# Optimization experiments

Hardware: AMD Instinct MI355X
Metric: run time of the kernel (lower is better)

## Reference

```python
import jax, jax.numpy as jnp
import numpy as np

EPS = 1e-6
NUM_HEADS = 8
FOCUS = 3.0


def setup_inputs() -> dict:
    key = jax.random.key(0)
    ks = jax.random.split(key, 8)
    B, N, C = 16, 4096, 256
    head_dim, ksz = C // NUM_HEADS, 5
    s = 1.0 / np.sqrt(C)
    return {
        "x": jax.random.normal(ks[0], (B, N, C), jnp.float32),
        "Wq": jax.random.normal(ks[1], (C, C), jnp.float32) * s,
        "Wkv": jax.random.normal(ks[2], (C, 2 * C), jnp.float32) * s,
        "Wp": jax.random.normal(ks[3], (C, C), jnp.float32) * s,
        "bp": jnp.zeros((C,), jnp.float32),
        "scale_param": jnp.zeros((1, 1, C), jnp.float32),
        "pos_enc": jax.random.normal(ks[4], (1, N, C), jnp.float32) * 0.02,
        "dwc_w": jax.random.normal(ks[5], (head_dim, 1, ksz, ksz), jnp.float32) * 0.1,
        "dwc_b": jnp.zeros((head_dim,), jnp.float32),
        "H": 64,
        "W": 64,
    }


def _focus(t, scale, f):
    # relu feature map + power focusing with norm restoration
    t = (jax.nn.relu(t) + EPS) / scale
    tn = jnp.linalg.norm(t, axis=-1, keepdims=True)
    tf = t ** f
    return tf / jnp.linalg.norm(tf, axis=-1, keepdims=True) * tn


def reference(x, Wq, Wkv, Wp, bp, scale_param, pos_enc, dwc_w, dwc_b, H, W):
    B, N, C = x.shape
    h = NUM_HEADS
    d = C // h
    n = N  # sr_ratio == 1

    q = x @ Wq                                  # [B,N,C]
    kv = x @ Wkv                                # [B,N,2C]
    k, v = kv[..., :C], kv[..., C:]
    k = k + pos_enc

    scale = jax.nn.softplus(scale_param)
    q = _focus(q, scale, FOCUS)
    k = _focus(k, scale, FOCUS)

    # split heads: [B,h,N,d]
    qh = q.reshape(B, N, h, d).transpose(0, 2, 1, 3)
    kh = k.reshape(B, n, h, d).transpose(0, 2, 1, 3)
    vh = v.reshape(B, n, h, d).transpose(0, 2, 1, 3)

    # linear attention: z = 1/(q . mean_n(k)), kv = k^T v / n, out = (q @ kv) * z
    z = 1.0 / (jnp.einsum("bhnd,bhd->bhn", qh, kh.mean(axis=2)) + EPS)
    kvmat = jnp.einsum("bhnd,bhne->bhde", kh, vh) / n     # [B,h,d,d]
    out = jnp.einsum("bhnd,bhde->bhne", qh, kvmat) * z[..., None]

    out = out.transpose(0, 2, 1, 3).reshape(B, N, C)      # [B,N,C]

    # depthwise conv on v over the HxW grid, per head-channel
    v4 = vh.reshape(B * h, H, W, d).transpose(0, 3, 1, 2)  # [B*h,d,H,W]
    conv = jax.lax.conv_general_dilated(
        v4, dwc_w, window_strides=(1, 1), padding="SAME",
        feature_group_count=d,
        dimension_numbers=("NCHW", "OIHW", "NCHW"))
    conv = conv + dwc_b[None, :, None, None]
    out = out + conv.reshape(B, C, N).transpose(0, 2, 1)

    return out @ Wp + bp
```

## Files before the change

kernel.cpp:

```cpp
#include <hip/hip_runtime.h>
#include <hip/hip_bf16.h>

typedef unsigned short u16;
using bf16_t = __hip_bfloat16;
typedef short short8 __attribute__((ext_vector_type(8)));
typedef float f32x4 __attribute__((ext_vector_type(4)));

__device__ __forceinline__ float b2f(u16 u) {
    return __uint_as_float((unsigned int)u << 16);
}
__device__ __forceinline__ u16 f2b(float f) {
    bf16_t h = __float2bfloat16(f);
    union { bf16_t h; u16 u; } cv; cv.h = h; return cv.u;
}
__device__ __forceinline__ float ldv(const void* p, size_t i, int f32) {
    return f32 ? ((const float*)p)[i] : b2f(((const u16*)p)[i]);
}
__device__ __forceinline__ uint4 pack8(float4 a, float4 b) {
    uint4 u;
    u.x = (unsigned)f2b(a.x) | ((unsigned)f2b(a.y) << 16);
    u.y = (unsigned)f2b(a.z) | ((unsigned)f2b(a.w) << 16);
    u.z = (unsigned)f2b(b.x) | ((unsigned)f2b(b.y) << 16);
    u.w = (unsigned)f2b(b.z) | ((unsigned)f2b(b.w) << 16);
    return u;
}
__device__ __forceinline__ int swz(int n, int k) {
    return k ^ ((n & 7) << 3);
}
__device__ __forceinline__ void gl16(const u16* g, u16* l) {
    __builtin_amdgcn_global_load_lds(
        (const __attribute__((address_space(1))) unsigned int*)g,
        (__attribute__((address_space(3))) unsigned int*)l, 16, 0, 0);
}

__global__ void detect_kernel(const void* __restrict__ x, int* __restrict__ flag)
{
    const int t = threadIdx.x;
    const u16 h = ((const u16*)x)[2 * t];
    const int e = (h >> 7) & 0xFF;
    const int plaus = (e >= 112 && e <= 133) ? 1 : 0;
    const unsigned long long m = __ballot(plaus);
    if (t == 0) flag[0] = (__popcll(m) < 32) ? 1 : 0;
}

__global__ __launch_bounds__(256)
void pecvt_kernel(const void* __restrict__ pe, u16* __restrict__ peb,
                  const int* __restrict__ flagp)
{
    const size_t i = ((size_t)blockIdx.x * 256 + threadIdx.x) * 4;
    if (*flagp) {
        const float4 f = *reinterpret_cast<const float4*>((const float*)pe + i);
        ushort4 o; o.x = f2b(f.x); o.y = f2b(f.y); o.z = f2b(f.z); o.w = f2b(f.w);
        *reinterpret_cast<ushort4*>(peb + i) = o;
    } else {
        *reinterpret_cast<ushort4*>(peb + i) =
            *reinterpret_cast<const ushort4*>((const u16*)pe + i);
    }
}

__global__ __launch_bounds__(256)
void wtrans_kernel(const void* __restrict__ W, u16* __restrict__ WT, int N,
                   const int* __restrict__ flagp)
{
    const int f32 = *flagp;
    __shared__ float tile[32][33];
    const int tx = threadIdx.x & 31, ty = threadIdx.x >> 5;
    const int bx = blockIdx.x % (N >> 5);
    const int by = blockIdx.x / (N >> 5);
    #pragma unroll
    for (int r = 0; r < 4; ++r) {
        const int k = by * 32 + ty + r * 8;
        const int n = bx * 32 + tx;
        tile[ty + r * 8][tx] = ldv(W, (size_t)k * N + n, f32);
    }
    __syncthreads();
    #pragma unroll
    for (int r = 0; r < 4; ++r) {
        const int n2 = bx * 32 + ty + r * 8;
        const int k2 = by * 32 + tx;
        WT[(size_t)n2 * 256 + k2] = f2b(tile[tx][ty + r * 8]);
    }
}

template<int MODE>
__global__ __launch_bounds__(256, 2)
void gemm256(const void* __restrict__ Aany, const u16* __restrict__ Abf,
             const u16* __restrict__ BT, u16* __restrict__ O0,
             const void* __restrict__ extra, const int* __restrict__ flagp)
{
    const int f32 = *flagp;
    __shared__ u16 As[128 * 64];
    __shared__ u16 Bs[256 * 64];
    __shared__ float red2[2][128];
    __shared__ float red6[2][128];
    __shared__ float ratio_s[128];
    __shared__ float sscr[256];

    const int tid  = threadIdx.x;
    const int row0 = blockIdx.x * 128;
    const int lane = tid & 63;
    const int wv   = tid >> 6;
    const int wvu  = __builtin_amdgcn_readfirstlane(wv);
    const int wm   = (wv & 1) * 64;
    const int wn   = (wv >> 1) * 128;
    const int l15  = lane & 15;
    const int lq   = lane >> 4;
    const int lr8  = lane >> 3;
    const int lc8  = (lane & 7) * 8;

    if (MODE == 3) {
        const float p = ldv(extra, tid, f32);
        const float s = (p > 20.f) ? p : log1pf(expf(p));
        sscr[tid] = 1.0f / s;
    }

    f32x4 acc[4][8] = {};

    for (int k0 = 0; k0 < 256; k0 += 64) {
        #pragma unroll
        for (int it = 0; it < 8; ++it) {
            const int r = wvu * 64 + it * 8 + lr8;
            gl16(BT + (size_t)r * 256 + k0 + swz(r, lc8),
                 &Bs[(wvu * 64 + it * 8) * 64]);
        }
        if (MODE == 2 || !f32) {
            const u16* Ab = (MODE == 2) ? Abf : (const u16*)Aany;
            #pragma unroll
            for (int it = 0; it < 4; ++it) {
                const int r = wvu * 32 + it * 8 + lr8;
                gl16(Ab + (size_t)(row0 + r) * 256 + k0 + swz(r, lc8),
                     &As[(wvu * 32 + it * 8) * 64]);
            }
        } else {
            const int sr = tid >> 1;
            const int sk = (tid & 1) * 32;
            const float* ag = (const float*)Aany +
                              (size_t)(row0 + sr) * 256 + k0 + sk;
            #pragma unroll
            for (int j = 0; j < 4; ++j) {
                const float4 f0 = *reinterpret_cast<const float4*>(ag + j * 8);
                const float4 f1 = *reinterpret_cast<const float4*>(ag + j * 8 + 4);
                *reinterpret_cast<uint4*>(
                    &As[sr * 64 + swz(sr, sk + j * 8)]) = pack8(f0, f1);
            }
        }
        __syncthreads();
        #pragma unroll
        for (int ks = 0; ks < 64; ks += 32) {
            const int ko = ks + lq * 8;
            short8 av[4], bv[8];
            #pragma unroll
            for (int i = 0; i < 4; ++i) {
                const int m = wm + i * 16 + l15;
                av[i] = *reinterpret_cast<const short8*>(&As[m * 64 + swz(m, ko)]);
            }
            #pragma unroll
            for (int j = 0; j < 8; ++j) {
                const int n = wn + j * 16 + l15;
                bv[j] = *reinterpret_cast<const short8*>(&Bs[n * 64 + swz(n, ko)]);
            }
            #pragma unroll
            for (int i = 0; i < 4; ++i)
                #pragma unroll
                for (int j = 0; j < 8; ++j)
                    acc[i][j] = __builtin_amdgcn_mfma_f32_16x16x32_bf16(
                        av[i], bv[j], acc[i][j], 0, 0, 0);
        }
        __syncthreads();
    }

    if (MODE == 3) {
        #pragma unroll
        for (int i = 0; i < 4; ++i) {
            #pragma unroll
            for (int rg = 0; rg < 4; ++rg) {
                const int lr = wm + i * 16 + lq * 4 + rg;
                float s2 = 0.f, s6 = 0.f;
                #pragma unroll
                for (int j = 0; j < 8; ++j) {
                    const int col = wn + j * 16 + l15;
                    const float xv =
                        (fmaxf(acc[i][j][rg], 0.f) + 1e-6f) * sscr[col];
                    acc[i][j][rg] = xv;
                    const float x2 = xv * xv;
                    s2 += x2;
                    s6 += x2 * x2 * x2;
                }
                #pragma unroll
                for (int off = 1; off < 16; off <<= 1) {
                    s2 += __shfl_xor(s2, off);
                    s6 += __shfl_xor(s6, off);
                }
                if (l15 == 0) { red2[wv >> 1][lr] = s2; red6[wv >> 1][lr] = s6; }
            }
        }
        __syncthreads();
        if (tid < 128)
            ratio_s[tid] = sqrtf((red2[0][tid] + red2[1][tid]) /
                                 (red6[0][tid] + red6[1][tid]));
        __syncthreads();
    }

    #pragma unroll
    for (int i = 0; i < 4; ++i) {
        #pragma unroll
        for (int j = 0; j < 8; ++j) {
            const int gcol = wn + j * 16 + l15;
            #pragma unroll
            for (int rg = 0; rg < 4; ++rg) {
                const int lr = wm + i * 16 + lq * 4 + rg;
                const size_t oi = (size_t)(row0 + lr) * 256 + gcol;
                const float a = acc[i][j][rg];
                if (MODE == 0) {
                    O0[oi] = f2b(a);
                } else if (MODE == 3) {
                    O0[oi] = f2b(a * a * a * ratio_s[lr]);
                } else {
                    const float o = a + ldv(extra, gcol, f32);
                    if (f32) ((float*)O0)[oi] = o;
                    else     O0[oi] = f2b(o);
                }
            }
        }
    }
}

__global__ __launch_bounds__(256, 2)
void fusedk_kernel(const void* __restrict__ x, const u16* __restrict__ WkvT,
                   const u16* __restrict__ peb, const u16* __restrict__ v,
                   const void* __restrict__ sp,
                   float* __restrict__ kvsm, float* __restrict__ ksm,
                   const int* __restrict__ flagp)
{
    const int f32 = *flagp;
    __shared__ u16 As[64 * 64];
    __shared__ u16 Bs[256 * 64];
    __shared__ u16 VsT[256 * 64];
    __shared__ float red2[4][64];
    __shared__ float red6[4][64];
    __shared__ float ratio_s[64];
    __shared__ float sscr[256];
    u16* KsT = Bs;

    const int tid  = threadIdx.x;
    const int lane = tid & 63;
    const int wv   = tid >> 6;
    const int wvu  = __builtin_amdgcn_readfirstlane(wv);
    const int l15  = lane & 15;
    const int lq   = lane >> 4;
    const int wn   = wv * 64;
    const int lr8  = lane >> 3;
    const int lc8  = (lane & 7) * 8;

    {
        const float p = ldv(sp, tid, f32);
        const float s = (p > 20.f) ? p : log1pf(expf(p));
        sscr[tid] = 1.0f / s;
    }

    f32x4 cc[2][4] = {};
    float ksp[4] = {0.f, 0.f, 0.f, 0.f};

    const int b   = blockIdx.x >> 5;
    const int vr  = lane;
    const int veb = wv * 64;

    for (int c = 0; c < 2; ++c) {
        const int row0 = blockIdx.x * 128 + c * 64;
        const int nb   = row0 & 4095;

        f32x4 acc[4][4] = {};
        for (int k0 = 0; k0 < 256; k0 += 64) {
            #pragma unroll
            for (int it = 0; it < 8; ++it) {
                const int r = wvu * 64 + it * 8 + lr8;
                gl16(WkvT + (size_t)r * 256 + k0 + swz(r, lc8),
                     &Bs[(wvu * 64 + it * 8) * 64]);
            }
            if (!f32) {
                #pragma unroll
                for (int it = 0; it < 2; ++it) {
                    const int r = wvu * 16 + it * 8 + lr8;
                    gl16((const u16*)x + (size_t)(row0 + r) * 256 + k0 + swz(r, lc8),
                         &As[(wvu * 16 + it * 8) * 64]);
                }
            } else {
                const int ar = tid >> 2, ak = (tid & 3) * 16;
                const float* ag = (const float*)x +
                                  (size_t)(row0 + ar) * 256 + k0 + ak;
                #pragma unroll
                for (int j = 0; j < 2; ++j) {
                    const float4 f0 = *reinterpret_cast<const float4*>(ag + j * 8);
                    const float4 f1 = *reinterpret_cast<const float4*>(ag + j * 8 + 4);
                    *reinterpret_cast<uint4*>(
                        &As[ar * 64 + swz(ar, ak + j * 8)]) = pack8(f0, f1);
                }
            }
            __syncthreads();
            #pragma unroll
            for (int ks = 0; ks < 64; ks += 32) {
                const int ko = ks + lq * 8;
                short8 av[4], bvv[4];
                #pragma unroll
                for (int i = 0; i < 4; ++i) {
                    const int m = i * 16 + l15;
                    av[i] = *reinterpret_cast<const short8*>(&As[m * 64 + swz(m, ko)]);
                }
                #pragma unroll
                for (int j = 0; j < 4; ++j) {
                    const int n = wn + j * 16 + l15;
                    bvv[j] = *reinterpret_cast<const short8*>(&Bs[n * 64 + swz(n, ko)]);
                }
                #pragma unroll
                for (int i = 0; i < 4; ++i)
                    #pragma unroll
                    for (int j = 0; j < 4; ++j)
                        acc[i][j] = __builtin_amdgcn_mfma_f32_16x16x32_bf16(
                            av[i], bvv[j], acc[i][j], 0, 0, 0);
            }
            __syncthreads();
        }

        #pragma unroll
        for (int i = 0; i < 4; ++i) {
            #pragma unroll
            for (int rg = 0; rg < 4; ++rg) {
                const int lrow = i * 16 + lq * 4 + rg;
                float s2 = 0.f, s6 = 0.f;
                #pragma unroll
                for (int j = 0; j < 4; ++j) {
                    const int col = wn + j * 16 + l15;
                    const float t = acc[i][j][rg] +
                        b2f(peb[(size_t)(nb + lrow) * 256 + col]);
                    const float xv = (fmaxf(t, 0.f) + 1e-6f) * sscr[col];
                    acc[i][j][rg] = xv;
                    const float x2 = xv * xv;
                    s2 += x2;
                    s6 += x2 * x2 * x2;
                }
                #pragma unroll
                for (int off = 1; off < 16; off <<= 1) {
                    s2 += __shfl_xor(s2, off);
                    s6 += __shfl_xor(s6, off);
                }
                if (l15 == 0) { red2[wv][lrow] = s2; red6[wv][lrow] = s6; }
            }
        }
        __syncthreads();
        if (tid < 64) {
            const float s2t = red2[0][tid] + red2[1][tid] + red2[2][tid] + red2[3][tid];
            const float s6t = red6[0][tid] + red6[1][tid] + red6[2][tid] + red6[3][tid];
            ratio_s[tid] = sqrtf(s2t / s6t);
        }
        __syncthreads();

        {
            float kscol[4] = {0.f, 0.f, 0.f, 0.f};
            #pragma unroll
            for (int i = 0; i < 4; ++i)
                #pragma unroll
                for (int rg = 0; rg < 4; ++rg) {
                    const int lrow = i * 16 + lq * 4 + rg;
                    const float rt = ratio_s[lrow];
                    #pragma unroll
                    for (int j = 0; j < 4; ++j) {
                        const float xv = acc[i][j][rg];
                        const float kf = xv * xv * xv * rt;
                        const int d = wn + j * 16 + l15;
                        KsT[d * 64 + swz(d, lrow)] = f2b(kf);
                        kscol[j] += kf;
                    }
                }
            #pragma unroll
            for (int j = 0; j < 4; ++j) {
                float kp = kscol[j];
                kp += __shfl_xor(kp, 16);
                kp += __shfl_xor(kp, 32);
                ksp[j] += kp;
            }
        }

        {
            const u16* vg = v + (size_t)(row0 + vr) * 256 + veb;
            uint4 t0[8];
            #pragma unroll
            for (int j = 0; j < 8; ++j)
                t0[j] = *reinterpret_cast<const uint4*>(vg + j * 8);
            #pragma unroll
            for (int j = 0; j < 8; ++j) {
                const u16* pp = (const u16*)&t0[j];
                #pragma unroll
                for (int m = 0; m < 8; ++m) {
                    const int e = veb + j * 8 + m;
                    VsT[e * 64 + swz(e, vr)] = pp[m];
                }
            }
        }
        __syncthreads();

        #pragma unroll
        for (int hh = 0; hh < 2; ++hh) {
            const int cb = (wv * 2 + hh) * 32;
            const int da = cb + l15, dbx = cb + 16 + l15;
            #pragma unroll
            for (int kk = 0; kk < 64; kk += 32) {
                const int ko = kk + lq * 8;
                const short8 a0 = *reinterpret_cast<const short8*>(
                    &KsT[da * 64 + swz(da, ko)]);
                const short8 a1 = *reinterpret_cast<const short8*>(
                    &KsT[dbx * 64 + swz(dbx, ko)]);
                const short8 b0 = *reinterpret_cast<const short8*>(
                    &VsT[da * 64 + swz(da, ko)]);
                const short8 b1 = *reinterpret_cast<const short8*>(
                    &VsT[dbx * 64 + swz(dbx, ko)]);
                cc[hh][0] = __builtin_amdgcn_mfma_f32_16x16x32_bf16(a0, b0, cc[hh][0], 0, 0, 0);
                cc[hh][1] = __builtin_amdgcn_mfma_f32_16x16x32_bf16(a0, b1, cc[hh][1], 0, 0, 0);
                cc[hh][2] = __builtin_amdgcn_mfma_f32_16x16x32_bf16(a1, b0, cc[hh][2], 0, 0, 0);
                cc[hh][3] = __builtin_amdgcn_mfma_f32_16x16x32_bf16(a1, b1, cc[hh][3], 0, 0, 0);
            }
        }
        __syncthreads();
    }

    const int slot = blockIdx.x & 1;
    float* ksb = ksm + (size_t)(slot * 16 + b) * 256;
    #pragma unroll
    for (int j = 0; j < 4; ++j)
        if (lane < 16)
            atomicAdd(&ksb[wn + j * 16 + lane], ksp[j]);
    #pragma unroll
    for (int hh = 0; hh < 2; ++hh) {
        const int h = wv * 2 + hh;
        float* base = kvsm + ((size_t)(slot * 16 + b) * 8 + h) * 1024;
        #pragma unroll
        for (int rg = 0; rg < 4; ++rg) {
            const int d0 = lq * 4 + rg;
            atomicAdd(&base[(size_t)d0 * 32 + l15],             cc[hh][0][rg]);
            atomicAdd(&base[(size_t)d0 * 32 + 16 + l15],        cc[hh][1][rg]);
            atomicAdd(&base[(size_t)(d0 + 16) * 32 + l15],      cc[hh][2][rg]);
            atomicAdd(&base[(size_t)(d0 + 16) * 32 + 16 + l15], cc[hh][3][rg]);
        }
    }
}

__global__ __launch_bounds__(256)
void attn_kernel(u16* qy, const float* __restrict__ kvsum,
                 const float* __restrict__ ksum)
{
    __shared__ float kvs[8][32][32];
    __shared__ float km[8][32];
    __shared__ float qs[16][256];
    const int tid = threadIdx.x;
    const int b   = blockIdx.x >> 8;
    const int n0  = (blockIdx.x & 255) * 16;
    const float inv_n = 1.0f / 4096.0f;
    for (int i = tid; i < 8 * 32 * 32; i += 256)
        (&kvs[0][0][0])[i] = (kvsum[(size_t)b * 8192 + i] +
                              kvsum[(size_t)(16 + b) * 8192 + i]) * inv_n;
    (&km[0][0])[tid] = (ksum[(size_t)b * 256 + tid] +
                        ksum[(size_t)(16 + b) * 256 + tid]) * inv_n;
    u16* qb = qy + ((size_t)b * 4096 + n0) * 256;
    #pragma unroll
    for (int t = 0; t < 16; ++t)
        qs[t][tid] = b2f(qb[(size_t)t * 256 + tid]);
    __syncthreads();
    const int h = tid >> 5, e = tid & 31;
    for (int t = 0; t < 16; ++t) {
        float acc = 0.f, zd = 0.f;
        #pragma unroll
        for (int d = 0; d < 32; ++d) {
            const float qv = qs[t][h * 32 + d];
            acc = fmaf(qv, kvs[h][d][e], acc);
            zd  = fmaf(qv, km[h][d], zd);
        }
        qb[(size_t)t * 256 + tid] = f2b(acc / (zd + 1e-6f));
    }
}

__global__ __launch_bounds__(256, 2)
void conv_add_kernel(const u16* __restrict__ v, const void* __restrict__ w,
                     const void* __restrict__ bias, u16* __restrict__ y,
                     const int* __restrict__ flagp)
{
    const int f32 = *flagp;
    __shared__ u16 vt[144 * 256];
    __shared__ float wl[800];
    __shared__ float bl[32];
    const int tid = threadIdx.x;
    for (int i = tid; i < 800; i += 256) wl[i] = ldv(w, i, f32);
    if (tid < 32) bl[tid] = ldv(bias, tid, f32);

    const int bb = blockIdx.x >> 6;
    const int ty = (blockIdx.x >> 3) & 7;
    const int tx = blockIdx.x & 7;
    const int y0 = ty * 8, x0 = tx * 8;
    const u16* vb = v + (size_t)bb * 4096 * 256;

    #pragma unroll
    for (int it = 0; it < 18; ++it) {
        const int idx = it * 256 + tid;
        const int px  = idx >> 5;
        const int c8  = (idx & 31) * 8;
        const int py  = px / 12, pxx = px - py * 12;
        const int yy = y0 + py - 2, xx = x0 + pxx - 2;
        uint4 val = {0u, 0u, 0u, 0u};
        if (yy >= 0 && yy < 64 && xx >= 0 && xx < 64)
            val = *reinterpret_cast<const uint4*>(
                vb + (size_t)((yy << 6) + xx) * 256 + c8);
        *reinterpret_cast<uint4*>(&vt[px * 256 + c8]) = val;
    }
    __syncthreads();

    const int c  = tid;
    const int dc = c & 31;
    float wreg[25];
    #pragma unroll
    for (int i = 0; i < 25; ++i) wreg[i] = wl[dc * 25 + i];
    const float bv = bl[dc];

    float win[5][12];
    #pragma unroll
    for (int r = 0; r < 5; ++r)
        #pragma unroll
        for (int cc = 0; cc < 12; ++cc)
            win[r][cc] = b2f(vt[(r * 12 + cc) * 256 + c]);

    u16* yb = y + ((size_t)bb * 4096 + (size_t)y0 * 64 + x0) * 256 + c;
    #pragma unroll
    for (int oy = 0; oy < 8; ++oy) {
        if (oy) {
            #pragma unroll
            for (int r = 0; r < 4; ++r)
                #pragma unroll
                for (int cc = 0; cc < 12; ++cc) win[r][cc] = win[r + 1][cc];
            #pragma unroll
            for (int cc = 0; cc < 12; ++cc)
                win[4][cc] = b2f(vt[((oy + 4) * 12 + cc) * 256 + c]);
        }
        #pragma unroll
        for (int ox = 0; ox < 8; ++ox) {
            float s = 0.f;
            #pragma unroll
            for (int ky = 0; ky < 5; ++ky)
                #pragma unroll
                for (int kx = 0; kx < 5; ++kx)
                    s = fmaf(win[ky][ox + kx], wreg[ky * 5 + kx], s);
            u16* yp = yb + (size_t)(oy * 64 + ox) * 256;
            *yp = f2b(b2f(*yp) + s + bv);
        }
    }
}

extern "C" void kernel_launch(void* const* d_in, const int* in_sizes, int n_in,
                              void* d_out, int out_size, void* d_ws, size_t ws_size,
                              hipStream_t stream)
{
    (void)in_sizes; (void)n_in; (void)out_size; (void)ws_size;
    const void* x   = d_in[0];
    const void* Wq  = d_in[1];
    const void* Wkv = d_in[2];
    const void* Wp  = d_in[3];
    const void* bp  = d_in[4];
    const void* sp  = d_in[5];
    const void* pe  = d_in[6];
    const void* dw  = d_in[7];
    const void* db  = d_in[8];

    int*   flag = (int*)d_ws;
    float* kvsm = (float*)((char*)d_ws + 64);
    float* ksm  = kvsm + 262144;
    u16*   WqT  = (u16*)(ksm + 8192);
    u16*   WkvT = WqT + 65536;
    u16*   WpT  = WkvT + 131072;
    u16*   peb  = WpT + 65536;
    u16*   qy   = peb + 1048576;
    u16*   v    = (u16*)d_out;

    hipMemsetAsync(kvsm, 0, (262144 + 8192) * sizeof(float), stream);
    detect_kernel<<<1, 64, 0, stream>>>(x, flag);
    pecvt_kernel<<<1024, 256, 0, stream>>>(pe, peb, flag);
    wtrans_kernel<<<64, 256, 0, stream>>>(Wq, WqT, 256, flag);
    wtrans_kernel<<<128, 256, 0, stream>>>(Wkv, WkvT, 512, flag);
    wtrans_kernel<<<64, 256, 0, stream>>>(Wp, WpT, 256, flag);

    hipLaunchKernelGGL((gemm256<3>), dim3(512), dim3(256), 0, stream,
                       x, (const u16*)nullptr, WqT, qy, sp, flag);
    hipLaunchKernelGGL((gemm256<0>), dim3(512), dim3(256), 0, stream,
                       x, (const u16*)nullptr, WkvT + (size_t)256 * 256, v,
                       (const void*)nullptr, flag);
    fusedk_kernel<<<512, 256, 0, stream>>>(x, WkvT, peb, v, sp, kvsm, ksm, flag);

    attn_kernel<<<4096, 256, 0, stream>>>(qy, kvsm, ksm);
    conv_add_kernel<<<1024, 256, 0, stream>>>(v, dw, db, qy, flag);
    hipLaunchKernelGGL((gemm256<2>), dim3(512), dim3(256), 0, stream,
                       (const void*)nullptr, qy, WpT, (u16*)d_out, bp, flag);
}
```

Before: 370.3 us.

## Pre-convert x to bf16 once and load K-projection tiles of 128 rows

Adds a conversion kernel that writes x to bf16 in the workspace, when the workspace is large enough. The three GEMMs that consume x then read it through the direct global-to-LDS bf16 path instead of each loading and packing fp32. fusedk_kernel now runs the K projection over all 128 rows in one k-loop, with two accumulator sets, instead of two passes over 64 rows each. Shared memory is aliased to fit the larger A tile. The extra pass writes 32MB of bf16, and the doubled accumulators raise register pressure.

```diff
diff --git a/kernel.cpp b/kernel.cpp
--- a/kernel.cpp
+++ b/kernel.cpp
@@ -41,6 +41,22 @@
     const int plaus = (e >= 112 && e <= 133) ? 1 : 0;
     const unsigned long long m = __ballot(plaus);
     if (t == 0) flag[0] = (__popcll(m) < 32) ? 1 : 0;
+}
+
+__global__ __launch_bounds__(256)
+void xcvt_kernel(const void* __restrict__ x, u16* __restrict__ xb,
+                 const int* __restrict__ flagp)
+{
+    const size_t i = ((size_t)blockIdx.x * 256 + threadIdx.x) * 8;
+    if (*flagp) {
+        const float* xf = (const float*)x + i;
+        const float4 f0 = *reinterpret_cast<const float4*>(xf);
+        const float4 f1 = *reinterpret_cast<const float4*>(xf + 4);
+        *reinterpret_cast<uint4*>(xb + i) = pack8(f0, f1);
+    } else {
+        *reinterpret_cast<uint4*>(xb + i) =
+            *reinterpret_cast<const uint4*>((const u16*)x + i);
+    }
 }
 
 __global__ __launch_bounds__(256)
@@ -86,7 +102,8 @@
 __global__ __launch_bounds__(256, 2)
 void gemm256(const void* __restrict__ Aany, const u16* __restrict__ Abf,
              const u16* __restrict__ BT, u16* __restrict__ O0,
-             const void* __restrict__ extra, const int* __restrict__ flagp)
+             const void* __restrict__ extra, const int* __restrict__ flagp,
+             int abf)
 {
     const int f32 = *flagp;
     __shared__ u16 As[128 * 64];
@@ -123,7 +140,7 @@
             gl16(BT + (size_t)r * 256 + k0 + swz(r, lc8),
                  &Bs[(wvu * 64 + it * 8) * 64]);
         }
-        if (MODE == 2 || !f32) {
+        if (MODE == 2 || abf || !f32) {
             const u16* Ab = (MODE == 2) ? Abf : (const u16*)Aany;
             #pragma unroll
             for (int it = 0; it < 4; ++it) {
@@ -230,17 +247,18 @@
                    const u16* __restrict__ peb, const u16* __restrict__ v,
                    const void* __restrict__ sp,
                    float* __restrict__ kvsm, float* __restrict__ ksm,
-                   const int* __restrict__ flagp)
+                   const int* __restrict__ flagp, int abf)
 {
     const int f32 = *flagp;
-    __shared__ u16 As[64 * 64];
-    __shared__ u16 Bs[256 * 64];
-    __shared__ u16 VsT[256 * 64];
+    __shared__ u16 smem[32768];
     __shared__ float red2[4][64];
     __shared__ float red6[4][64];
     __shared__ float ratio_s[64];
     __shared__ float sscr[256];
-    u16* KsT = Bs;
+    u16* As  = smem;
+    u16* Bs  = smem + 8192;
+    u16* KsT = smem;
+    u16* VsT = smem + 16384;
 
     const int tid  = threadIdx.x;
     const int lane = tid & 63;
@@ -261,49 +279,49 @@
     f32x4 cc[2][4] = {};
     float ksp[4] = {0.f, 0.f, 0.f, 0.f};
 
-    const int b   = blockIdx.x >> 5;
-    const int vr  = lane;
-    const int veb = wv * 64;
-
-    for (int c = 0; c < 2; ++c) {
-        const int row0 = blockIdx.x * 128 + c * 64;
-        const int nb   = row0 & 4095;
-
-        f32x4 acc[4][4] = {};
-        for (int k0 = 0; k0 < 256; k0 += 64) {
-            #pragma unroll
-            for (int it = 0; it < 8; ++it) {
-                const int r = wvu * 64 + it * 8 + lr8;
-                gl16(WkvT + (size_t)r * 256 + k0 + swz(r, lc8),
-                     &Bs[(wvu * 64 + it * 8) * 64]);
-            }
-            if (!f32) {
-                #pragma unroll
-                for (int it = 0; it < 2; ++it) {
-                    const int r = wvu * 16 + it * 8 + lr8;
-                    gl16((const u16*)x + (size_t)(row0 + r) * 256 + k0 + swz(r, lc8),
-                         &As[(wvu * 16 + it * 8) * 64]);
-                }
-            } else {
-                const int ar = tid >> 2, ak = (tid & 3) * 16;
-                const float* ag = (const float*)x +
-                                  (size_t)(row0 + ar) * 256 + k0 + ak;
-                #pragma unroll
-                for (int j = 0; j < 2; ++j) {
-                    const float4 f0 = *reinterpret_cast<const float4*>(ag + j * 8);
-                    const float4 f1 = *reinterpret_cast<const float4*>(ag + j * 8 + 4);
-                    *reinterpret_cast<uint4*>(
-                        &As[ar * 64 + swz(ar, ak + j * 8)]) = pack8(f0, f1);
-                }
-            }
-            __syncthreads();
+    const int b    = blockIdx.x >> 5;
+    const int row0 = blockIdx.x * 128;
+    const int vr   = lane;
+    const int veb  = wv * 64;
+
+    f32x4 acc[2][4][4] = {};
+    for (int k0 = 0; k0 < 256; k0 += 64) {
+        #pragma unroll
+        for (int it = 0; it < 8; ++it) {
+            const int r = wvu * 64 + it * 8 + lr8;
+            gl16(WkvT + (size_t)r * 256 + k0 + swz(r, lc8),
+                 &Bs[(wvu * 64 + it * 8) * 64]);
+        }
+        if (abf || !f32) {
+            #pragma unroll
+            for (int it = 0; it < 4; ++it) {
+                const int r = wvu * 32 + it * 8 + lr8;
+                gl16((const u16*)x + (size_t)(row0 + r) * 256 + k0 + swz(r, lc8),
+                     &As[(wvu * 32 + it * 8) * 64]);
+            }
+        } else {
+            const int sr = tid >> 1;
+            const int sk = (tid & 1) * 32;
+            const float* ag = (const float*)x +
+                              (size_t)(row0 + sr) * 256 + k0 + sk;
+            #pragma unroll
+            for (int j = 0; j < 4; ++j) {
+                const float4 f0 = *reinterpret_cast<const float4*>(ag + j * 8);
+                const float4 f1 = *reinterpret_cast<const float4*>(ag + j * 8 + 4);
+                *reinterpret_cast<uint4*>(
+                    &As[sr * 64 + swz(sr, sk + j * 8)]) = pack8(f0, f1);
+            }
+        }
+        __syncthreads();
+        #pragma unroll
+        for (int c = 0; c < 2; ++c) {
             #pragma unroll
             for (int ks = 0; ks < 64; ks += 32) {
                 const int ko = ks + lq * 8;
                 short8 av[4], bvv[4];
                 #pragma unroll
                 for (int i = 0; i < 4; ++i) {
-                    const int m = i * 16 + l15;
+                    const int m = c * 64 + i * 16 + l15;
                     av[i] = *reinterpret_cast<const short8*>(&As[m * 64 + swz(m, ko)]);
                 }
                 #pragma unroll
@@ -315,11 +333,16 @@
                 for (int i = 0; i < 4; ++i)
                     #pragma unroll
                     for (int j = 0; j < 4; ++j)
-                        acc[i][j] = __builtin_amdgcn_mfma_f32_16x16x32_bf16(
-                            av[i], bvv[j], acc[i][j], 0, 0, 0);
-            }
-            __syncthreads();
-        }
+                        acc[c][i][j] = __builtin_amdgcn_mfma_f32_16x16x32_bf16(
+                            av[i], bvv[j], acc[c][i][j], 0, 0, 0);
+            }
+        }
+        __syncthreads();
+    }
+
+    #pragma unroll
+    for (int c = 0; c < 2; ++c) {
+        const int nb = (row0 & 4095) + c * 64;
 
         #pragma unroll
         for (int i = 0; i < 4; ++i) {
@@ -330,10 +353,10 @@
                 #pragma unroll
                 for (int j = 0; j < 4; ++j) {
                     const int col = wn + j * 16 + l15;
-                    const float t = acc[i][j][rg] +
+                    const float t = acc[c][i][j][rg] +
                         b2f(peb[(size_t)(nb + lrow) * 256 + col]);
                     const float xv = (fmaxf(t, 0.f) + 1e-6f) * sscr[col];
-                    acc[i][j][rg] = xv;
+                    acc[c][i][j][rg] = xv;
                     const float x2 = xv * xv;
                     s2 += x2;
                     s6 += x2 * x2 * x2;
@@ -364,7 +387,7 @@
                     const float rt = ratio_s[lrow];
                     #pragma unroll
                     for (int j = 0; j < 4; ++j) {
-                        const float xv = acc[i][j][rg];
+                        const float xv = acc[c][i][j][rg];
                         const float kf = xv * xv * xv * rt;
                         const int d = wn + j * 16 + l15;
                         KsT[d * 64 + swz(d, lrow)] = f2b(kf);
@@ -381,7 +404,7 @@
         }
 
         {
-            const u16* vg = v + (size_t)(row0 + vr) * 256 + veb;
+            const u16* vg = v + (size_t)(row0 + c * 64 + vr) * 256 + veb;
             uint4 t0[8];
             #pragma unroll
             for (int j = 0; j < 8; ++j)
@@ -555,7 +578,7 @@
                               void* d_out, int out_size, void* d_ws, size_t ws_size,
                               hipStream_t stream)
 {
-    (void)in_sizes; (void)n_in; (void)out_size; (void)ws_size;
+    (void)in_sizes; (void)n_in; (void)out_size;
     const void* x   = d_in[0];
     const void* Wq  = d_in[1];
     const void* Wkv = d_in[2];
@@ -574,24 +597,32 @@
     u16*   WpT  = WkvT + 131072;
     u16*   peb  = WpT + 65536;
     u16*   qy   = peb + 1048576;
+    u16*   xb   = qy + (size_t)16777216;
     u16*   v    = (u16*)d_out;
+
+    const size_t need = (size_t)((char*)(xb + 16777216) - (char*)d_ws);
+    const int big = (ws_size >= need) ? 1 : 0;
 
     hipMemsetAsync(kvsm, 0, (262144 + 8192) * sizeof(float), stream);
     detect_kernel<<<1, 64, 0, stream>>>(x, flag);
+    if (big) xcvt_kernel<<<8192, 256, 0, stream>>>(x, xb, flag);
     pecvt_kernel<<<1024, 256, 0, stream>>>(pe, peb, flag);
     wtrans_kernel<<<64, 256, 0, stream>>>(Wq, WqT, 256, flag);
     wtrans_kernel<<<128, 256, 0, stream>>>(Wkv, WkvT, 512, flag);
     wtrans_kernel<<<64, 256, 0, stream>>>(Wp, WpT, 256, flag);
 
+    const void* Ax = big ? (const void*)xb : x;
+
     hipLaunchKernelGGL((gemm256<3>), dim3(512), dim3(256), 0, stream,
-                       x, (const u16*)nullptr, WqT, qy, sp, flag);
+                       Ax, (const u16*)nullptr, WqT, qy, sp, flag, big);
     hipLaunchKernelGGL((gemm256<0>), dim3(512), dim3(256), 0, stream,
-                       x, (const u16*)nullptr, WkvT + (size_t)256 * 256, v,
-                       (const void*)nullptr, flag);
-    fusedk_kernel<<<512, 256, 0, stream>>>(x, WkvT, peb, v, sp, kvsm, ksm, flag);
+                       Ax, (const u16*)nullptr, WkvT + (size_t)256 * 256, v,
+                       (const void*)nullptr, flag, big);
+    fusedk_kernel<<<512, 256, 0, stream>>>(Ax, WkvT, peb, v, sp, kvsm, ksm,
+                                           flag, big);
 
     attn_kernel<<<4096, 256, 0, stream>>>(qy, kvsm, ksm);
     conv_add_kernel<<<1024, 256, 0, stream>>>(v, dw, db, qy, flag);
     hipLaunchKernelGGL((gemm256<2>), dim3(512), dim3(256), 0, stream,
-                       (const void*)nullptr, qy, WpT, (u16*)d_out, bp, flag);
-}
+                       (const void*)nullptr, qy, WpT, (u16*)d_out, bp, flag, 0);
+}
```

New measurement: 358.6 us. 3.2% less time.
